# Optimization experiments

Hardware: AMD Instinct MI355X
Metric: run time of the kernel (lower is better)

Reference implementation:

```python
import jax, jax.numpy as jnp
import numpy as np

B, T, N, C_IN, C_OUT, D_E, GH, H = 16, 12, 2048, 64, 64, 16, 32, 4


def setup_inputs() -> dict:
    key = jax.random.key(0)
    ks = jax.random.split(key, 12)
    f = jax.random.normal
    return {
        "x": f(ks[0], (B, T, N, C_IN), jnp.float32),
        "init_state": jnp.zeros((B, N, C_OUT), jnp.float32),
        "node_embeddings": f(ks[1], (N, D_E), jnp.float32),
        "gat_W": f(ks[2], (H, D_E, GH), jnp.float32) * 0.3,
        "gat_a_src": f(ks[3], (H, GH), jnp.float32) * 0.3,
        "gat_a_dst": f(ks[4], (H, GH), jnp.float32) * 0.3,
        "wp_gates": f(ks[5], (D_E, 2, C_IN + C_OUT, 2 * C_OUT), jnp.float32) * 0.05,
        "bp_gates": f(ks[6], (D_E, 2 * C_OUT), jnp.float32) * 0.05,
        "wp_cand": f(ks[7], (D_E, 2, C_IN + C_OUT, C_OUT), jnp.float32) * 0.05,
        "bp_cand": f(ks[8], (D_E, C_OUT), jnp.float32) * 0.05,
        "tc_w": f(ks[9], (C_OUT, C_OUT, 1, 3), jnp.float32) * 0.05,
        "tc_b": jnp.zeros((C_OUT,), jnp.float32),
        "rc_w": f(ks[10], (C_OUT, C_IN, 1, 1), jnp.float32) * 0.05,
        "rc_b": jnp.zeros((C_OUT,), jnp.float32),
        "ln_g": jnp.ones((C_OUT,), jnp.float32),
        "ln_b": jnp.zeros((C_OUT,), jnp.float32),
    }


def _forward(x, init_state, node_embeddings, gat_W, gat_a_src, gat_a_dst,
             wp_gates, bp_gates, wp_cand, bp_cand, tc_w, tc_b, rc_w, rc_b, ln_g, ln_b):
    E = node_embeddings
    # GAT-style adaptive support over node embeddings: [N, N]
    h = jnp.einsum('nd,hdf->hnf', E, gat_W)                       # [H,N,GH]
    s = jnp.einsum('hnf,hf->hn', h, gat_a_src)
    d = jnp.einsum('hnf,hf->hn', h, gat_a_dst)
    e = jax.nn.leaky_relu(s[:, :, None] + d[:, None, :], 0.2)     # [H,N,N]
    A = jax.nn.softmax(e, axis=-1).mean(0)                        # [N,N]
    # node-adaptive weights (NAL): per-node weights from embedding pools
    W_g = jnp.einsum('nd,dkio->nkio', E, wp_gates)                # [N,2,Cin+Cout,2Cout]
    b_g = E @ bp_gates                                            # [N,2Cout]
    W_c = jnp.einsum('nd,dkio->nkio', E, wp_cand)
    b_c = E @ bp_cand

    def gconv(inp, W, b):
        # cheb order-2 supports [I, A] over inp: [B,N,C] -> [B,N,out]
        xg = jnp.stack([inp, jnp.einsum('mn,bnc->bmc', A, inp)], 2)
        return jnp.einsum('bnki,nkio->bno', xg, W) + b

    def step(state, xt):
        zr = jax.nn.sigmoid(gconv(jnp.concatenate([xt, state], -1), W_g, b_g))
        z, r = jnp.split(zr, 2, axis=-1)
        hc = jnp.tanh(gconv(jnp.concatenate([xt, r * state], -1), W_c, b_c))
        new = z * state + (1.0 - z) * hc
        return new, new

    last, inner = jax.lax.scan(step, init_state, jnp.swapaxes(x, 0, 1))
    inner = jnp.swapaxes(inner, 0, 1)                             # [B,T,N,C]

    cur = jnp.transpose(inner, (0, 3, 2, 1))                      # [B,C,N,T]
    tco = jax.lax.conv_general_dilated(
        cur, tc_w, (1, 1), [(0, 0), (1, 1)],
        dimension_numbers=('NCHW', 'OIHW', 'NCHW')) + tc_b[None, :, None, None]
    xp = jnp.transpose(x, (0, 3, 2, 1))                           # [B,Cin,N,T]
    res = jnp.einsum('oc,bcnt->bont', rc_w[:, :, 0, 0], xp) + rc_b[None, :, None, None]
    y = jnp.transpose(jax.nn.relu(res + tco), (0, 3, 2, 1))       # [B,T,N,C]
    mu = y.mean(-1, keepdims=True)
    var = y.var(-1, keepdims=True)
    y = (y - mu) / jnp.sqrt(var + 1e-5) * ln_g + ln_b
    return y, last


def reference(x, init_state, node_embeddings, gat_W, gat_a_src, gat_a_dst,
              wp_gates, bp_gates, wp_cand, bp_cand, tc_w, tc_b, rc_w, rc_b, ln_g, ln_b):
    y, last = _forward(x, init_state, node_embeddings, gat_W, gat_a_src, gat_a_dst,
                       wp_gates, bp_gates, wp_cand, bp_cand, tc_w, tc_b, rc_w, rc_b, ln_g, ln_b)
    return (y, last)
```

## Files before the change

### kernel.cpp

```cpp
#include <hip/hip_runtime.h>
#include <stdint.h>

#define B_  16
#define T_  12
#define N_  2048
#define DE_ 16
#define GH_ 32
#define NH_ 4

typedef __attribute__((ext_vector_type(8)))  short short8;
typedef __attribute__((ext_vector_type(4)))  float f32x4;
typedef __attribute__((ext_vector_type(16))) float f32x16;

__device__ __forceinline__ unsigned short f2b(float f){
  unsigned u = __float_as_uint(f);
  return (unsigned short)((u + 0x7fffu + ((u>>16)&1u)) >> 16);
}
__device__ __forceinline__ float b2f(unsigned short h){
  return __uint_as_float(((unsigned)h)<<16);
}
__device__ __forceinline__ unsigned pk2(float a, float b){
  return (unsigned)f2b(a) | ((unsigned)f2b(b)<<16);
}
__device__ __forceinline__ float lrelu(float v){ return v>=0.f ? v : 0.2f*v; }

__device__ __forceinline__ void gl16(const void* g, void* l){
  __builtin_amdgcn_global_load_lds((const __attribute__((address_space(1))) void*)g,
                                   (__attribute__((address_space(3))) void*)l, 16, 0, 0);
}

__global__ __launch_bounds__(256) void k_gat_sd(const float* __restrict__ E, const float* __restrict__ gW,
    const float* __restrict__ asrc, const float* __restrict__ adst,
    float* __restrict__ sArr, float* __restrict__ dArr)
{
  int id = blockIdx.x*256 + threadIdx.x;
  int h = id >> 11, n = id & 2047;
  float hv[GH_];
#pragma unroll
  for (int f=0; f<GH_; ++f) hv[f]=0.f;
  for (int d=0; d<DE_; ++d){
    float e = E[n*DE_+d];
    const float* wr = gW + (h*DE_+d)*GH_;
#pragma unroll
    for (int f=0; f<GH_; ++f) hv[f] += e*wr[f];
  }
  float s=0.f, dd=0.f;
#pragma unroll
  for (int f=0; f<GH_; ++f){ s += hv[f]*asrc[h*GH_+f]; dd += hv[f]*adst[h*GH_+f]; }
  sArr[h*N_+n]=s; dArr[h*N_+n]=dd;
}

__global__ __launch_bounds__(256) void k_dmax(const float* __restrict__ dArr, float* __restrict__ dmax){
  __shared__ float red[256];
  int h = blockIdx.x, t = threadIdx.x;
  float m = -1e30f;
  for (int i=t;i<N_;i+=256) m = fmaxf(m, dArr[h*N_+i]);
  red[t]=m; __syncthreads();
  for (int s=128;s>0;s>>=1){ if (t<s) red[t]=fmaxf(red[t],red[t+s]); __syncthreads(); }
  if (t==0) dmax[h]=red[0];
}

__global__ __launch_bounds__(256) void k_denom(const float* __restrict__ sArr, const float* __restrict__ dArr,
                                               const float* __restrict__ dmax, float* __restrict__ denom){
  __shared__ float red[256];
  int m = blockIdx.x, h = blockIdx.y, t = threadIdx.x;
  float sm = sArr[h*N_+m];
  float shift = lrelu(sm + dmax[h]);
  float acc=0.f;
  for (int i=t;i<N_;i+=256) acc += __expf(lrelu(sm + dArr[h*N_+i]) - shift);
  red[t]=acc; __syncthreads();
  for (int s=128;s>0;s>>=1){ if (t<s) red[t]+=red[t+s]; __syncthreads(); }
  if (t==0) denom[h*N_+m]=red[0];
}

__global__ __launch_bounds__(256) void k_adj(const float* __restrict__ sArr, const float* __restrict__ dArr,
                                             const float* __restrict__ dmax, const float* __restrict__ denom,
                                             unsigned short* __restrict__ Abf){
  int m = blockIdx.x, t = threadIdx.x;
  float sm[NH_], sh[NH_], inv[NH_];
#pragma unroll
  for (int h=0;h<NH_;++h){ sm[h]=sArr[h*N_+m]; sh[h]=lrelu(sm[h]+dmax[h]); inv[h]=1.f/denom[h*N_+m]; }
  for (int n=t;n<N_;n+=256){
    float acc=0.f;
#pragma unroll
    for (int h=0;h<NH_;++h) acc += __expf(lrelu(sm[h]+dArr[h*N_+n]) - sh[h]) * inv[h];
    Abf[(long)m*N_+n] = f2b(acc*0.25f);
  }
}

__global__ __launch_bounds__(256) void k_nalw(const float* __restrict__ E, const float* __restrict__ wp,
                                              unsigned short* __restrict__ Wout, int Osz){
  __shared__ float sS[256][17];
  __shared__ float sE[512*16];
  int o = blockIdx.x, q = blockIdx.y, t = threadIdx.x;
  int slot = t>>3, j = t&7;
  int kio = (((slot ^ (o&7))&31)<<3) | j;
  long dstride = 256L*Osz;
  for (int d=0; d<DE_; ++d) sS[t][d] = wp[d*dstride + (long)kio*Osz + o];
  for (int i=t; i<512*16; i+=256) sE[i] = E[q*512*16 + i];
  __syncthreads();
  unsigned short* out = Wout + (long)(q*512)*dstride + o*256 + t;
  for (int nn=0; nn<512; ++nn){
    float acc=0.f;
    const float* e = &sE[nn*16];
#pragma unroll
    for (int d=0; d<DE_; ++d) acc += e[d]*sS[t][d];
    out[(long)nn*dstride] = f2b(acc);
  }
}

__global__ __launch_bounds__(256) void k_nalb(const float* __restrict__ E, const float* __restrict__ bpg,
                                              const float* __restrict__ bpc,
                                              unsigned short* __restrict__ bg, unsigned short* __restrict__ bc){
  int id = blockIdx.x*256+threadIdx.x;
  int n = id/192, oo = id%192;
  float acc=0.f;
  if (oo<128){
    for (int d=0;d<DE_;++d) acc += E[n*DE_+d]*bpg[d*128+oo];
    bg[n*128+oo]=f2b(acc);
  } else {
    int c=oo-128;
    for (int d=0;d<DE_;++d) acc += E[n*DE_+d]*bpc[d*64+c];
    bc[n*64+c]=f2b(acc);
  }
}

__global__ __launch_bounds__(256) void k_wcat(const float* __restrict__ tcw, const float* __restrict__ rcw,
                                              unsigned short* __restrict__ Wcat){
  int id = blockIdx.x*256+threadIdx.x;
  int o = id>>8, k = id&255;
  float v;
  if (k<192){ int dt=k>>6, c=k&63; v = tcw[(o*64+c)*3+dt]; }
  else v = rcw[o*64 + (k&63)];
  int pos = o*256 + ((((k>>3)&31) ^ (o&7))<<3) + (k&7);
  Wcat[pos] = f2b(v);
}

__global__ __launch_bounds__(256) void k_init(const float* __restrict__ init, float* __restrict__ st,
                                              unsigned short* __restrict__ stb){
  int i = blockIdx.x*256+threadIdx.x;
  float v = init[i]; st[i]=v; stb[i]=f2b(v);
}

template<int BM, int BN, bool F32SRC>
__global__ __launch_bounds__(256) void k_gemm(
    const unsigned short* __restrict__ Abf,
    const char* __restrict__ S0, long ss0,
    const char* __restrict__ S1, long ss1,
    unsigned short* __restrict__ D0, long ds0,
    unsigned short* __restrict__ D1, long ds1)
{
  constexpr int BK=64;
  constexpr int IA = BM/32;
  constexpr int WTM = BM/2, WTN = BN/2;
  constexpr int MTC = WTM/32, NTC = WTN/32;
  __shared__ __align__(16) unsigned short sA[BM*BK];
  __shared__ __align__(16) unsigned short sB[BN*BK];
  int tid = threadIdx.x, w = tid>>6, l = tid&63;
  int mB = blockIdx.x, z = blockIdx.y;
  const char* s0 = S0 + (long)z*ss0;
  const char* s1 = (BN==128) ? (S1 + (long)z*ss1) : (const char*)0;
  int wm = w&1, wn = w>>1;
  f32x16 acc[MTC][NTC];
#pragma unroll
  for (int a=0;a<MTC;++a)
#pragma unroll
    for (int b=0;b<NTC;++b)
#pragma unroll
      for (int i=0;i<16;++i) acc[a][b][i]=0.f;

  constexpr int JG = BN/4;
  int jg = tid & (JG-1), kg = tid / JG;
  bool bact = (kg < 8);
  int j0 = jg*4, k0 = kg*8;

  for (int kb=0; kb<2048/BK; ++kb){
    __syncthreads();
#pragma unroll
    for (int i=0;i<IA;++i){
      int c = (w*IA+i)*64 + l;
      int row = c>>3, slot = c&7;
      int g = slot ^ (row&7);
      gl16((const char*)Abf + (((long)(mB*BM+row))*2048 + kb*BK + g*8)*2,
           (char*)sA + (w*IA+i)*1024);
    }
    if (bact){
      unsigned short vv[8][4];
#pragma unroll
      for (int ii=0; ii<8; ++ii){
        int k = kb*BK + k0 + ii;
        const char* sp; int jj0;
        if (BN==128 && j0>=64){ sp = s1; jj0 = j0-64; } else { sp = s0; jj0 = j0; }
        if (F32SRC){
          const float4 v = *(const float4*)(sp + ((long)k*64 + jj0)*4);
          vv[ii][0]=f2b(v.x); vv[ii][1]=f2b(v.y); vv[ii][2]=f2b(v.z); vv[ii][3]=f2b(v.w);
        } else {
          const ushort4 v = *(const ushort4*)(sp + ((long)k*64 + jj0)*2);
          vv[ii][0]=v.x; vv[ii][1]=v.y; vv[ii][2]=v.z; vv[ii][3]=v.w;
        }
      }
#pragma unroll
      for (int r=0;r<4;++r){
        int jj = j0 + r;
        uint4 pkv;
        pkv.x = (unsigned)vv[0][r] | ((unsigned)vv[1][r]<<16);
        pkv.y = (unsigned)vv[2][r] | ((unsigned)vv[3][r]<<16);
        pkv.z = (unsigned)vv[4][r] | ((unsigned)vv[5][r]<<16);
        pkv.w = (unsigned)vv[6][r] | ((unsigned)vv[7][r]<<16);
        *(uint4*)((char*)sB + jj*128 + ((kg ^ (jj&7))<<4)) = pkv;
      }
    }
    __syncthreads();
#pragma unroll
    for (int ks=0; ks<BK/16; ++ks){
      short8 af[MTC];
#pragma unroll
      for (int mt=0; mt<MTC; ++mt){
        int row = wm*WTM + mt*32 + (l&31);
        int g = ks*2 + (l>>5);
        af[mt] = *(const short8*)((const char*)sA + row*128 + ((g ^ (row&7))<<4));
      }
#pragma unroll
      for (int nt=0; nt<NTC; ++nt){
        int jj = wn*WTN + nt*32 + (l&31);
        int g = ks*2 + (l>>5);
        short8 bfv = *(const short8*)((const char*)sB + jj*128 + ((g ^ (jj&7))<<4));
#pragma unroll
        for (int mt=0; mt<MTC; ++mt)
          acc[mt][nt] = __builtin_amdgcn_mfma_f32_32x32x16_bf16(af[mt], bfv, acc[mt][nt], 0,0,0);
      }
    }
  }
  unsigned short* d0 = D0 + (long)z*ds0;
  unsigned short* d1 = (BN==128) ? (D1 + (long)z*ds1) : (unsigned short*)0;
#pragma unroll
  for (int mt=0; mt<MTC; ++mt)
#pragma unroll
    for (int nt=0; nt<NTC; ++nt)
#pragma unroll
      for (int rg=0; rg<16; ++rg){
        int rl = wm*WTM + mt*32 + (rg&3) + 8*(rg>>2) + 4*(l>>5);
        int col = wn*WTN + nt*32 + (l&31);
        long m = (long)mB*BM + rl;
        unsigned short v = f2b(acc[mt][nt][rg]);
        if (BN==128 && col>=64) d1[m*64 + (col-64)] = v;
        else d0[m*64 + col] = v;
      }
}

__global__ __launch_bounds__(256) void k_gates(
    const float* __restrict__ x, const float* __restrict__ st,
    const unsigned short* __restrict__ AX, const unsigned short* __restrict__ AS,
    const unsigned short* __restrict__ Wg, const unsigned short* __restrict__ bg,
    float* __restrict__ zbuf, unsigned short* __restrict__ rs, int t)
{
  __shared__ __align__(16) unsigned short sW[64*256];
  __shared__ __align__(16) unsigned short sX[16*256];
  int n = blockIdx.x, half = blockIdx.y;
  int tid = threadIdx.x, w = tid>>6, l = tid&63;
  const unsigned short* Wsrc = Wg + (long)n*32768 + half*16384;
#pragma unroll
  for (int i=0;i<8;++i){
    int c = (w*8+i)*64 + l;
    gl16((const char*)Wsrc + c*16, (char*)sW + (w*8+i)*1024);
  }
  int b = tid>>4, c16 = tid&15;
  uint4 g0, g1;
  if (c16 < 8){
    const float* p = (c16<4) ? (x  + (((long)(b*T_+t)*N_ + n)*64 + c16*16))
                             : (st + (((long)b*N_ + n)*64 + (c16-4)*16));
    float4 f0 = *(const float4*)(p+0), f1 = *(const float4*)(p+4);
    float4 f2v = *(const float4*)(p+8), f3 = *(const float4*)(p+12);
    g0.x = pk2(f0.x,f0.y); g0.y = pk2(f0.z,f0.w); g0.z = pk2(f1.x,f1.y); g0.w = pk2(f1.z,f1.w);
    g1.x = pk2(f2v.x,f2v.y); g1.y = pk2(f2v.z,f2v.w); g1.z = pk2(f3.x,f3.y); g1.w = pk2(f3.z,f3.w);
  } else {
    const unsigned short* p = (c16<12) ? (AX + (((long)(b*T_+t)*N_ + n)*64 + (c16-8)*16))
                                       : (AS + (((long)b*N_ + n)*64 + (c16-12)*16));
    g0 = *(const uint4*)(p); g1 = *(const uint4*)(p+8);
  }
  {
    int gg = c16*2;
    *(uint4*)((char*)sX + b*512 + (((gg  ) ^ (b&7))<<4)) = g0;
    *(uint4*)((char*)sX + b*512 + (((gg+1) ^ (b&7))<<4)) = g1;
  }
  __syncthreads();
  f32x4 acc; 
#pragma unroll
  for (int i=0;i<4;++i) acc[i]=0.f;
  int orow = w*16 + (l&15);
  int arow = l&15;
#pragma unroll
  for (int ks=0; ks<8; ++ks){
    int g = ks*4 + (l>>4);
    short8 a = *(const short8*)((const char*)sX + arow*512 + ((g ^ (arow&7))<<4));
    short8 bb = *(const short8*)((const char*)sW + orow*512 + ((g ^ (orow&7))<<4));
    acc = __builtin_amdgcn_mfma_f32_16x16x32_bf16(a, bb, acc, 0,0,0);
  }
  int o = half*64 + orow;
  float bia = b2f(bg[n*128 + o]);
#pragma unroll
  for (int i=0;i<4;++i){
    int bb2 = (l>>4)*4 + i;
    float v = acc[i] + bia;
    float sg = 1.f/(1.f+__expf(-v));
    long idx = ((long)bb2*N_ + n)*64;
    if (half==0) zbuf[idx + o] = sg;
    else {
      float s0v = st[idx + (o-64)];
      rs[idx + (o-64)] = f2b(sg*s0v);
    }
  }
}

__global__ __launch_bounds__(256) void k_cand(
    const float* __restrict__ x, const float* __restrict__ zbuf,
    const unsigned short* __restrict__ AX, const unsigned short* __restrict__ ARS,
    const unsigned short* __restrict__ rs,
    const unsigned short* __restrict__ Wc, const unsigned short* __restrict__ bc,
    float* __restrict__ st, unsigned short* __restrict__ stb,
    unsigned short* __restrict__ inner, int t)
{
  __shared__ __align__(16) unsigned short sW[64*256];
  __shared__ __align__(16) unsigned short sX[16*256];
  int n = blockIdx.x;
  int tid = threadIdx.x, w = tid>>6, l = tid&63;
  const unsigned short* Wsrc = Wc + (long)n*16384;
#pragma unroll
  for (int i=0;i<8;++i){
    int c = (w*8+i)*64 + l;
    gl16((const char*)Wsrc + c*16, (char*)sW + (w*8+i)*1024);
  }
  int b = tid>>4, c16 = tid&15;
  uint4 g0, g1;
  if (c16 < 4){
    const float* p = x + (((long)(b*T_+t)*N_ + n)*64 + c16*16);
    float4 f0 = *(const float4*)(p+0), f1 = *(const float4*)(p+4);
    float4 f2v = *(const float4*)(p+8), f3 = *(const float4*)(p+12);
    g0.x = pk2(f0.x,f0.y); g0.y = pk2(f0.z,f0.w); g0.z = pk2(f1.x,f1.y); g0.w = pk2(f1.z,f1.w);
    g1.x = pk2(f2v.x,f2v.y); g1.y = pk2(f2v.z,f2v.w); g1.z = pk2(f3.x,f3.y); g1.w = pk2(f3.z,f3.w);
  } else {
    const unsigned short* p;
    if (c16<8)       p = rs  + (((long)b*N_ + n)*64 + (c16-4)*16);
    else if (c16<12) p = AX  + (((long)(b*T_+t)*N_ + n)*64 + (c16-8)*16);
    else             p = ARS + (((long)b*N_ + n)*64 + (c16-12)*16);
    g0 = *(const uint4*)(p); g1 = *(const uint4*)(p+8);
  }
  {
    int gg = c16*2;
    *(uint4*)((char*)sX + b*512 + (((gg  ) ^ (b&7))<<4)) = g0;
    *(uint4*)((char*)sX + b*512 + (((gg+1) ^ (b&7))<<4)) = g1;
  }
  __syncthreads();
  f32x4 acc;
#pragma unroll
  for (int i=0;i<4;++i) acc[i]=0.f;
  int orow = w*16 + (l&15);
  int arow = l&15;
#pragma unroll
  for (int ks=0; ks<8; ++ks){
    int g = ks*4 + (l>>4);
    short8 a = *(const short8*)((const char*)sX + arow*512 + ((g ^ (arow&7))<<4));
    short8 bb = *(const short8*)((const char*)sW + orow*512 + ((g ^ (orow&7))<<4));
    acc = __builtin_amdgcn_mfma_f32_16x16x32_bf16(a, bb, acc, 0,0,0);
  }
  float bia = b2f(bc[n*64 + orow]);
#pragma unroll
  for (int i=0;i<4;++i){
    int bb2 = (l>>4)*4 + i;
    float hc = tanhf(acc[i] + bia);
    long idx = ((long)bb2*N_ + n)*64 + orow;
    float zv = zbuf[idx];
    float olds = st[idx];
    float nv = zv*olds + (1.f-zv)*hc;
    st[idx]=nv; stb[idx]=f2b(nv);
    inner[((long)(bb2*T_+t)*N_ + n)*64 + orow] = f2b(nv);
  }
}

__global__ __launch_bounds__(256) void k_post(
    const unsigned short* __restrict__ inner, const float* __restrict__ x,
    const unsigned short* __restrict__ Wcat,
    const float* __restrict__ tcb, const float* __restrict__ rcb,
    const float* __restrict__ lng, const float* __restrict__ lnb,
    float* __restrict__ out)
{
  __shared__ __align__(16) unsigned short sF[64*256];
  __shared__ __align__(16) unsigned short sW[64*256];
  int id = blockIdx.x;
  int bt = id>>5, nb = id&31;
  int b = bt/T_, t = bt%T_;
  int n0 = nb*64;
  int tid = threadIdx.x, w = tid>>6, l = tid&63;
#pragma unroll
  for (int i=0;i<8;++i){
    int c = (w*8+i)*64 + l;
    gl16((const char*)Wcat + c*16, (char*)sW + (w*8+i)*1024);
  }
  int row = tid&63, q = tid>>6;
  uint4 ch[8];
  if (q<3){
    int ts = t + q - 1;
    if (ts>=0 && ts<T_){
      const uint4* p = (const uint4*)(inner + (((long)(b*T_+ts)*N_) + n0+row)*64);
#pragma unroll
      for (int hh=0;hh<8;++hh) ch[hh]=p[hh];
    } else {
      uint4 zz; zz.x=0u; zz.y=0u; zz.z=0u; zz.w=0u;
#pragma unroll
      for (int hh=0;hh<8;++hh) ch[hh]=zz;
    }
  } else {
    const float4* p = (const float4*)(x + (((long)bt*N_) + n0+row)*64);
#pragma unroll
    for (int hh=0;hh<8;++hh){
      float4 u0=p[2*hh], u1=p[2*hh+1];
      ch[hh].x=pk2(u0.x,u0.y); ch[hh].y=pk2(u0.z,u0.w);
      ch[hh].z=pk2(u1.x,u1.y); ch[hh].w=pk2(u1.z,u1.w);
    }
  }
#pragma unroll
  for (int hh=0;hh<8;++hh){
    int g = q*8+hh;
    *(uint4*)((char*)sF + row*512 + ((g ^ (row&7))<<4)) = ch[hh];
  }
  __syncthreads();
  f32x4 acc[4];
#pragma unroll
  for (int ot=0; ot<4; ++ot)
#pragma unroll
    for (int i=0;i<4;++i) acc[ot][i]=0.f;
  int arow = w*16 + (l&15);
#pragma unroll
  for (int ks=0; ks<8; ++ks){
    int g = ks*4 + (l>>4);
    short8 a = *(const short8*)((const char*)sF + arow*512 + ((g ^ (arow&7))<<4));
#pragma unroll
    for (int ot=0; ot<4; ++ot){
      int o = ot*16 + (l&15);
      short8 bb = *(const short8*)((const char*)sW + o*512 + ((g ^ (o&7))<<4));
      acc[ot] = __builtin_amdgcn_mfma_f32_16x16x32_bf16(a, bb, acc[ot], 0,0,0);
    }
  }
  float s1[4]={0.f,0.f,0.f,0.f}, s2[4]={0.f,0.f,0.f,0.f};
#pragma unroll
  for (int ot=0; ot<4; ++ot){
    int o = ot*16 + (l&15);
    float bia = tcb[o] + rcb[o];
#pragma unroll
    for (int i=0;i<4;++i){
      float v = fmaxf(acc[ot][i] + bia, 0.f);
      acc[ot][i] = v;
      s1[i]+=v; s2[i]+=v*v;
    }
  }
#pragma unroll
  for (int msk=1; msk<16; msk<<=1){
#pragma unroll
    for (int i=0;i<4;++i){
      s1[i] += __shfl_xor(s1[i], msk, 64);
      s2[i] += __shfl_xor(s2[i], msk, 64);
    }
  }
#pragma unroll
  for (int i=0;i<4;++i){
    float mu = s1[i]*(1.f/64.f);
    float var = s2[i]*(1.f/64.f) - mu*mu;
    float rstd = rsqrtf(fmaxf(var,0.f)+1e-5f);
    int rr = n0 + w*16 + (l>>4)*4 + i;
#pragma unroll
    for (int ot=0; ot<4; ++ot){
      int o = ot*16 + (l&15);
      out[(((long)bt*N_) + rr)*64 + o] = (acc[ot][i]-mu)*rstd*lng[o] + lnb[o];
    }
  }
}

extern "C" void kernel_launch(void* const* d_in, const int* in_sizes, int n_in,
                              void* d_out, int out_size, void* d_ws, size_t ws_size,
                              hipStream_t stream)
{
  const float* x    = (const float*)d_in[0];
  const float* init = (const float*)d_in[1];
  const float* E    = (const float*)d_in[2];
  const float* gW   = (const float*)d_in[3];
  const float* asrc = (const float*)d_in[4];
  const float* adst = (const float*)d_in[5];
  const float* wpg  = (const float*)d_in[6];
  const float* bpg  = (const float*)d_in[7];
  const float* wpc  = (const float*)d_in[8];
  const float* bpc  = (const float*)d_in[9];
  const float* tcw  = (const float*)d_in[10];
  const float* tcb  = (const float*)d_in[11];
  const float* rcw  = (const float*)d_in[12];
  const float* rcb  = (const float*)d_in[13];
  const float* lng  = (const float*)d_in[14];
  const float* lnb  = (const float*)d_in[15];
  float* out = (float*)d_out;

  char* p = (char*)d_ws;
  auto alloc = [&](size_t bytes)->char*{ char* r = p; p += (bytes + 255) & ~(size_t)255; return r; };
  unsigned short* Abf  = (unsigned short*)alloc((size_t)N_*N_*2);
  unsigned short* Wg   = (unsigned short*)alloc((size_t)N_*32768*2);
  unsigned short* Wc   = (unsigned short*)alloc((size_t)N_*16384*2);
  unsigned short* bg   = (unsigned short*)alloc((size_t)N_*128*2);
  unsigned short* bc   = (unsigned short*)alloc((size_t)N_*64*2);
  unsigned short* AX   = (unsigned short*)alloc((size_t)B_*T_*N_*64*2);
  unsigned short* AS   = (unsigned short*)alloc((size_t)B_*N_*64*2);
  unsigned short* ARS  = (unsigned short*)alloc((size_t)B_*N_*64*2);
  unsigned short* rsb  = (unsigned short*)alloc((size_t)B_*N_*64*2);
  unsigned short* stb  = (unsigned short*)alloc((size_t)B_*N_*64*2);
  unsigned short* inner= (unsigned short*)alloc((size_t)B_*T_*N_*64*2);
  unsigned short* Wcat = (unsigned short*)alloc((size_t)64*256*2);
  float* sArr = (float*)alloc((size_t)NH_*N_*4);
  float* dArr = (float*)alloc((size_t)NH_*N_*4);
  float* dmax = (float*)alloc((size_t)NH_*4);
  float* denom= (float*)alloc((size_t)NH_*N_*4);
  float* stf  = (float*)alloc((size_t)B_*N_*64*4);
  float* zbuf = (float*)alloc((size_t)B_*N_*64*4);

  k_gat_sd<<<32,256,0,stream>>>(E,gW,asrc,adst,sArr,dArr);
  k_dmax<<<4,256,0,stream>>>(dArr,dmax);
  k_denom<<<dim3(N_,NH_),256,0,stream>>>(sArr,dArr,dmax,denom);
  k_adj<<<N_,256,0,stream>>>(sArr,dArr,dmax,denom,Abf);
  k_nalw<<<dim3(128,4),256,0,stream>>>(E,wpg,Wg,128);
  k_nalw<<<dim3(64,4),256,0,stream>>>(E,wpc,Wc,64);
  k_nalb<<<1536,256,0,stream>>>(E,bpg,bpc,bg,bc);
  k_wcat<<<64,256,0,stream>>>(tcw,rcw,Wcat);
  k_init<<<(B_*N_*64)/256,256,0,stream>>>(init,stf,stb);

  k_gemm<128,128,true><<<dim3(16,96),256,0,stream>>>(Abf,
      (const char*)x,          2L*N_*64*4,
      (const char*)(x + N_*64),2L*N_*64*4,
      AX,          2L*N_*64,
      AX + N_*64,  2L*N_*64);

  for (int t=0; t<T_; ++t){
    k_gemm<64,64,false><<<dim3(32,16),256,0,stream>>>(Abf,
        (const char*)stb, (long)N_*64*2, (const char*)0, 0,
        AS, (long)N_*64, (unsigned short*)0, 0);
    k_gates<<<dim3(N_,2),256,0,stream>>>(x,stf,AX,AS,Wg,bg,zbuf,rsb,t);
    k_gemm<64,64,false><<<dim3(32,16),256,0,stream>>>(Abf,
        (const char*)rsb, (long)N_*64*2, (const char*)0, 0,
        ARS, (long)N_*64, (unsigned short*)0, 0);
    k_cand<<<N_,256,0,stream>>>(x,zbuf,AX,ARS,rsb,Wc,bc,stf,stb,inner,t);
  }

  k_post<<<B_*T_*32,256,0,stream>>>(inner,x,Wcat,tcb,rcb,lng,lnb,out);
  hipMemcpyAsync(out + (size_t)B_*T_*N_*64, stf, (size_t)B_*N_*64*4,
                 hipMemcpyDeviceToDevice, stream);
}
```

Measured before the change: 2.073 ms.

## Pre-swizzle GEMM B operands so A·X GEMMs load B tiles directly

Adds a pre-pass that converts x to bf16 in a k-blocked, XOR-swizzled layout. The state and reset-state producers now also write that layout, so the adjacency GEMMs can fetch B tiles with direct 16-byte global-to-LDS loads instead of doing per-thread transposes and conversions. The GEMM outputs switch to a node-major layout with all batches side by side, so one wide GEMM covers all B*T or B columns. Blocks are also remapped so that neighbouring M tiles land on the same XCD. In exchange there are extra buffers, an extra swizzled write of rs, and scattered stores in the gate and candidate epilogues.

```diff
diff --git a/kernel.cpp b/kernel.cpp
--- a/kernel.cpp
+++ b/kernel.cpp
@@ -86,6 +86,37 @@
     for (int h=0;h<NH_;++h) acc += __expf(lrelu(sm[h]+dArr[h*N_+n]) - sh[h]) * inv[h];
     Abf[(long)m*N_+n] = f2b(acc*0.25f);
   }
+}
+
+__global__ __launch_bounds__(256) void k_xsw(const float* __restrict__ x,
+                                             unsigned short* __restrict__ xsw)
+{
+  __shared__ unsigned short sT[256*64];
+  int kb = blockIdx.x;
+  int btB = blockIdx.y;
+  int tid = threadIdx.x;
+  int btl = tid>>6, kin = tid&63;
+  int n  = kb*64 + kin;
+  int bt = btB*4 + btl;
+  const float* src = x + ((long)bt*N_ + n)*64;
+  unsigned short row[64];
+#pragma unroll
+  for (int c4=0; c4<16; ++c4){
+    float4 v = *(const float4*)(src + c4*4);
+    row[c4*4+0]=f2b(v.x); row[c4*4+1]=f2b(v.y); row[c4*4+2]=f2b(v.z); row[c4*4+3]=f2b(v.w);
+  }
+  int g0 = kin>>3, e = kin&7;
+#pragma unroll
+  for (int c=0; c<64; ++c){
+    int jl = btl*64 + c;
+    int s = g0 ^ (c&7);
+    sT[jl*64 + s*8 + e] = row[c];
+  }
+  __syncthreads();
+  unsigned short* dst = xsw + ((long)kb*12288 + btB*256)*64;
+  const uint4* sp = (const uint4*)sT;
+  uint4* dp = (uint4*)dst;
+  for (int i=tid; i<2048; i+=256) dp[i] = sp[i];
 }
 
 __global__ __launch_bounds__(256) void k_nalw(const float* __restrict__ E, const float* __restrict__ wp,
@@ -136,30 +167,35 @@
   Wcat[pos] = f2b(v);
 }
 
-__global__ __launch_bounds__(256) void k_init(const float* __restrict__ init, float* __restrict__ st,
-                                              unsigned short* __restrict__ stb){
+__global__ __launch_bounds__(256) void k_init2(const float* __restrict__ init, float* __restrict__ st,
+                                               unsigned short* __restrict__ stb){
   int i = blockIdx.x*256+threadIdx.x;
-  float v = init[i]; st[i]=v; stb[i]=f2b(v);
-}
-
-template<int BM, int BN, bool F32SRC>
-__global__ __launch_bounds__(256) void k_gemm(
-    const unsigned short* __restrict__ Abf,
-    const char* __restrict__ S0, long ss0,
-    const char* __restrict__ S1, long ss1,
-    unsigned short* __restrict__ D0, long ds0,
-    unsigned short* __restrict__ D1, long ds1)
-{
-  constexpr int BK=64;
-  constexpr int IA = BM/32;
+  float v = init[i]; st[i]=v;
+  int c = i&63, n = (i>>6)&2047, b = i>>17;
+  int kb = n>>6, kin = n&63;
+  int j = b*64 + c;
+  int s = (kin>>3) ^ (c&7);
+  stb[((long)kb*1024 + j)*64 + s*8 + (kin&7)] = f2b(v);
+}
+
+template<int BM, int BN, int JTOT>
+__global__ __launch_bounds__(256) void k_gemm2(
+    const unsigned short* __restrict__ A,
+    const unsigned short* __restrict__ Bs,
+    unsigned short* __restrict__ D)
+{
+  constexpr int MBLK = 2048/BM, MPX = MBLK/8;
+  constexpr int NIA = BM*64*2/(256*16);
+  constexpr int NIB = BN*64*2/(256*16);
   constexpr int WTM = BM/2, WTN = BN/2;
   constexpr int MTC = WTM/32, NTC = WTN/32;
-  __shared__ __align__(16) unsigned short sA[BM*BK];
-  __shared__ __align__(16) unsigned short sB[BN*BK];
+  __shared__ __align__(16) unsigned short sA[BM*64];
+  __shared__ __align__(16) unsigned short sB[BN*64];
+  int bid = blockIdx.x;
+  int xcd = bid & 7, idx = bid >> 3;
+  int mB = xcd*MPX + (idx % MPX);
+  int jB = idx / MPX;
   int tid = threadIdx.x, w = tid>>6, l = tid&63;
-  int mB = blockIdx.x, z = blockIdx.y;
-  const char* s0 = S0 + (long)z*ss0;
-  const char* s1 = (BN==128) ? (S1 + (long)z*ss1) : (const char*)0;
   int wm = w&1, wn = w>>1;
   f32x16 acc[MTC][NTC];
 #pragma unroll
@@ -169,70 +205,39 @@
 #pragma unroll
       for (int i=0;i<16;++i) acc[a][b][i]=0.f;
 
-  constexpr int JG = BN/4;
-  int jg = tid & (JG-1), kg = tid / JG;
-  bool bact = (kg < 8);
-  int j0 = jg*4, k0 = kg*8;
-
-  for (int kb=0; kb<2048/BK; ++kb){
+  for (int kb=0; kb<32; ++kb){
     __syncthreads();
 #pragma unroll
-    for (int i=0;i<IA;++i){
-      int c = (w*IA+i)*64 + l;
-      int row = c>>3, slot = c&7;
-      int g = slot ^ (row&7);
-      gl16((const char*)Abf + (((long)(mB*BM+row))*2048 + kb*BK + g*8)*2,
-           (char*)sA + (w*IA+i)*1024);
-    }
-    if (bact){
-      unsigned short vv[8][4];
-#pragma unroll
-      for (int ii=0; ii<8; ++ii){
-        int k = kb*BK + k0 + ii;
-        const char* sp; int jj0;
-        if (BN==128 && j0>=64){ sp = s1; jj0 = j0-64; } else { sp = s0; jj0 = j0; }
-        if (F32SRC){
-          const float4 v = *(const float4*)(sp + ((long)k*64 + jj0)*4);
-          vv[ii][0]=f2b(v.x); vv[ii][1]=f2b(v.y); vv[ii][2]=f2b(v.z); vv[ii][3]=f2b(v.w);
-        } else {
-          const ushort4 v = *(const ushort4*)(sp + ((long)k*64 + jj0)*2);
-          vv[ii][0]=v.x; vv[ii][1]=v.y; vv[ii][2]=v.z; vv[ii][3]=v.w;
-        }
-      }
-#pragma unroll
-      for (int r=0;r<4;++r){
-        int jj = j0 + r;
-        uint4 pkv;
-        pkv.x = (unsigned)vv[0][r] | ((unsigned)vv[1][r]<<16);
-        pkv.y = (unsigned)vv[2][r] | ((unsigned)vv[3][r]<<16);
-        pkv.z = (unsigned)vv[4][r] | ((unsigned)vv[5][r]<<16);
-        pkv.w = (unsigned)vv[6][r] | ((unsigned)vv[7][r]<<16);
-        *(uint4*)((char*)sB + jj*128 + ((kg ^ (jj&7))<<4)) = pkv;
-      }
-    }
+    for (int i=0;i<NIA;++i){
+      int c = (w*NIA+i)*64 + l;
+      int row = c>>3, slot = c&7, g = slot ^ (row&7);
+      gl16((const char*)A + (((long)(mB*BM+row))*2048 + kb*64 + g*8)*2,
+           (char*)sA + (w*NIA+i)*1024);
+    }
+    const char* bt = (const char*)(Bs + ((long)kb*JTOT + jB*BN)*64);
+#pragma unroll
+    for (int i=0;i<NIB;++i)
+      gl16(bt + ((w*NIB+i)*64 + l)*16, (char*)sB + (w*NIB+i)*1024);
     __syncthreads();
 #pragma unroll
-    for (int ks=0; ks<BK/16; ++ks){
+    for (int ks=0; ks<4; ++ks){
+      int gk = ks*2 + (l>>5);
       short8 af[MTC];
 #pragma unroll
       for (int mt=0; mt<MTC; ++mt){
         int row = wm*WTM + mt*32 + (l&31);
-        int g = ks*2 + (l>>5);
-        af[mt] = *(const short8*)((const char*)sA + row*128 + ((g ^ (row&7))<<4));
+        af[mt] = *(const short8*)((const char*)sA + row*128 + ((gk ^ (row&7))<<4));
       }
 #pragma unroll
       for (int nt=0; nt<NTC; ++nt){
         int jj = wn*WTN + nt*32 + (l&31);
-        int g = ks*2 + (l>>5);
-        short8 bfv = *(const short8*)((const char*)sB + jj*128 + ((g ^ (jj&7))<<4));
+        short8 bfv = *(const short8*)((const char*)sB + jj*128 + ((gk ^ (jj&7))<<4));
 #pragma unroll
         for (int mt=0; mt<MTC; ++mt)
           acc[mt][nt] = __builtin_amdgcn_mfma_f32_32x32x16_bf16(af[mt], bfv, acc[mt][nt], 0,0,0);
       }
     }
   }
-  unsigned short* d0 = D0 + (long)z*ds0;
-  unsigned short* d1 = (BN==128) ? (D1 + (long)z*ds1) : (unsigned short*)0;
 #pragma unroll
   for (int mt=0; mt<MTC; ++mt)
 #pragma unroll
@@ -240,19 +245,18 @@
 #pragma unroll
       for (int rg=0; rg<16; ++rg){
         int rl = wm*WTM + mt*32 + (rg&3) + 8*(rg>>2) + 4*(l>>5);
-        int col = wn*WTN + nt*32 + (l&31);
+        int col = jB*BN + wn*WTN + nt*32 + (l&31);
         long m = (long)mB*BM + rl;
-        unsigned short v = f2b(acc[mt][nt][rg]);
-        if (BN==128 && col>=64) d1[m*64 + (col-64)] = v;
-        else d0[m*64 + col] = v;
+        D[m*JTOT + col] = f2b(acc[mt][nt][rg]);
       }
 }
 
 __global__ __launch_bounds__(256) void k_gates(
     const float* __restrict__ x, const float* __restrict__ st,
-    const unsigned short* __restrict__ AX, const unsigned short* __restrict__ AS,
+    const unsigned short* __restrict__ AXn, const unsigned short* __restrict__ AS,
     const unsigned short* __restrict__ Wg, const unsigned short* __restrict__ bg,
-    float* __restrict__ zbuf, unsigned short* __restrict__ rs, int t)
+    float* __restrict__ zbuf, unsigned short* __restrict__ rsp,
+    unsigned short* __restrict__ rsb, int t)
 {
   __shared__ __align__(16) unsigned short sW[64*256];
   __shared__ __align__(16) unsigned short sX[16*256];
@@ -274,8 +278,9 @@
     g0.x = pk2(f0.x,f0.y); g0.y = pk2(f0.z,f0.w); g0.z = pk2(f1.x,f1.y); g0.w = pk2(f1.z,f1.w);
     g1.x = pk2(f2v.x,f2v.y); g1.y = pk2(f2v.z,f2v.w); g1.z = pk2(f3.x,f3.y); g1.w = pk2(f3.z,f3.w);
   } else {
-    const unsigned short* p = (c16<12) ? (AX + (((long)(b*T_+t)*N_ + n)*64 + (c16-8)*16))
-                                       : (AS + (((long)b*N_ + n)*64 + (c16-12)*16));
+    const unsigned short* p = (c16<12)
+      ? (AXn + ((long)n*12288 + (b*T_+t)*64 + (c16-8)*16))
+      : (AS  + ((long)n*1024  + b*64       + (c16-12)*16));
     g0 = *(const uint4*)(p); g1 = *(const uint4*)(p+8);
   }
   {
@@ -284,7 +289,7 @@
     *(uint4*)((char*)sX + b*512 + (((gg+1) ^ (b&7))<<4)) = g1;
   }
   __syncthreads();
-  f32x4 acc; 
+  f32x4 acc;
 #pragma unroll
   for (int i=0;i<4;++i) acc[i]=0.f;
   int orow = w*16 + (l&15);
@@ -298,24 +303,28 @@
   }
   int o = half*64 + orow;
   float bia = b2f(bg[n*128 + o]);
+  int kb = n>>6, kin = n&63;
+  int sw = (kin>>3) ^ (orow&7);
 #pragma unroll
   for (int i=0;i<4;++i){
-    int bb2 = (l>>4)*4 + i;
+    int b2 = (l>>4)*4 + i;
     float v = acc[i] + bia;
     float sg = 1.f/(1.f+__expf(-v));
-    long idx = ((long)bb2*N_ + n)*64;
+    long idx = ((long)b2*N_ + n)*64;
     if (half==0) zbuf[idx + o] = sg;
     else {
-      float s0v = st[idx + (o-64)];
-      rs[idx + (o-64)] = f2b(sg*s0v);
+      float s0v = st[idx + orow];
+      unsigned short rv = f2b(sg*s0v);
+      rsp[idx + orow] = rv;
+      rsb[((long)kb*1024 + b2*64 + orow)*64 + sw*8 + (kin&7)] = rv;
     }
   }
 }
 
 __global__ __launch_bounds__(256) void k_cand(
     const float* __restrict__ x, const float* __restrict__ zbuf,
-    const unsigned short* __restrict__ AX, const unsigned short* __restrict__ ARS,
-    const unsigned short* __restrict__ rs,
+    const unsigned short* __restrict__ AXn, const unsigned short* __restrict__ ARS,
+    const unsigned short* __restrict__ rsp,
     const unsigned short* __restrict__ Wc, const unsigned short* __restrict__ bc,
     float* __restrict__ st, unsigned short* __restrict__ stb,
     unsigned short* __restrict__ inner, int t)
@@ -340,9 +349,9 @@
     g1.x = pk2(f2v.x,f2v.y); g1.y = pk2(f2v.z,f2v.w); g1.z = pk2(f3.x,f3.y); g1.w = pk2(f3.z,f3.w);
   } else {
     const unsigned short* p;
-    if (c16<8)       p = rs  + (((long)b*N_ + n)*64 + (c16-4)*16);
-    else if (c16<12) p = AX  + (((long)(b*T_+t)*N_ + n)*64 + (c16-8)*16);
-    else             p = ARS + (((long)b*N_ + n)*64 + (c16-12)*16);
+    if (c16<8)       p = rsp + (((long)b*N_ + n)*64 + (c16-4)*16);
+    else if (c16<12) p = AXn + ((long)n*12288 + (b*T_+t)*64 + (c16-8)*16);
+    else             p = ARS + ((long)n*1024  + b*64       + (c16-12)*16);
     g0 = *(const uint4*)(p); g1 = *(const uint4*)(p+8);
   }
   {
@@ -364,16 +373,20 @@
     acc = __builtin_amdgcn_mfma_f32_16x16x32_bf16(a, bb, acc, 0,0,0);
   }
   float bia = b2f(bc[n*64 + orow]);
+  int kb = n>>6, kin = n&63;
+  int sw = (kin>>3) ^ (orow&7);
 #pragma unroll
   for (int i=0;i<4;++i){
-    int bb2 = (l>>4)*4 + i;
+    int b2 = (l>>4)*4 + i;
     float hc = tanhf(acc[i] + bia);
-    long idx = ((long)bb2*N_ + n)*64 + orow;
+    long idx = ((long)b2*N_ + n)*64 + orow;
     float zv = zbuf[idx];
     float olds = st[idx];
     float nv = zv*olds + (1.f-zv)*hc;
-    st[idx]=nv; stb[idx]=f2b(nv);
-    inner[((long)(bb2*T_+t)*N_ + n)*64 + orow] = f2b(nv);
+    st[idx]=nv;
+    unsigned short nb = f2b(nv);
+    stb[((long)kb*1024 + b2*64 + orow)*64 + sw*8 + (kin&7)] = nb;
+    inner[((long)(b2*T_+t)*N_ + n)*64 + orow] = nb;
   }
 }
 
@@ -504,11 +517,13 @@
   unsigned short* Wc   = (unsigned short*)alloc((size_t)N_*16384*2);
   unsigned short* bg   = (unsigned short*)alloc((size_t)N_*128*2);
   unsigned short* bc   = (unsigned short*)alloc((size_t)N_*64*2);
-  unsigned short* AX   = (unsigned short*)alloc((size_t)B_*T_*N_*64*2);
-  unsigned short* AS   = (unsigned short*)alloc((size_t)B_*N_*64*2);
-  unsigned short* ARS  = (unsigned short*)alloc((size_t)B_*N_*64*2);
-  unsigned short* rsb  = (unsigned short*)alloc((size_t)B_*N_*64*2);
-  unsigned short* stb  = (unsigned short*)alloc((size_t)B_*N_*64*2);
+  unsigned short* xsw  = (unsigned short*)alloc((size_t)N_*12288*2);
+  unsigned short* AXn  = (unsigned short*)alloc((size_t)N_*12288*2);
+  unsigned short* AS   = (unsigned short*)alloc((size_t)N_*1024*2);
+  unsigned short* ARS  = (unsigned short*)alloc((size_t)N_*1024*2);
+  unsigned short* rsb  = (unsigned short*)alloc((size_t)N_*1024*2);
+  unsigned short* rsp  = (unsigned short*)alloc((size_t)N_*1024*2);
+  unsigned short* stb  = (unsigned short*)alloc((size_t)N_*1024*2);
   unsigned short* inner= (unsigned short*)alloc((size_t)B_*T_*N_*64*2);
   unsigned short* Wcat = (unsigned short*)alloc((size_t)64*256*2);
   float* sArr = (float*)alloc((size_t)NH_*N_*4);
@@ -522,27 +537,20 @@
   k_dmax<<<4,256,0,stream>>>(dArr,dmax);
   k_denom<<<dim3(N_,NH_),256,0,stream>>>(sArr,dArr,dmax,denom);
   k_adj<<<N_,256,0,stream>>>(sArr,dArr,dmax,denom,Abf);
+  k_xsw<<<dim3(32,48),256,0,stream>>>(x,xsw);
   k_nalw<<<dim3(128,4),256,0,stream>>>(E,wpg,Wg,128);
   k_nalw<<<dim3(64,4),256,0,stream>>>(E,wpc,Wc,64);
   k_nalb<<<1536,256,0,stream>>>(E,bpg,bpc,bg,bc);
   k_wcat<<<64,256,0,stream>>>(tcw,rcw,Wcat);
-  k_init<<<(B_*N_*64)/256,256,0,stream>>>(init,stf,stb);
-
-  k_gemm<128,128,true><<<dim3(16,96),256,0,stream>>>(Abf,
-      (const char*)x,          2L*N_*64*4,
-      (const char*)(x + N_*64),2L*N_*64*4,
-      AX,          2L*N_*64,
-      AX + N_*64,  2L*N_*64);
+  k_init2<<<(B_*N_*64)/256,256,0,stream>>>(init,stf,stb);
+
+  k_gemm2<128,128,12288><<<1536,256,0,stream>>>(Abf, xsw, AXn);
 
   for (int t=0; t<T_; ++t){
-    k_gemm<64,64,false><<<dim3(32,16),256,0,stream>>>(Abf,
-        (const char*)stb, (long)N_*64*2, (const char*)0, 0,
-        AS, (long)N_*64, (unsigned short*)0, 0);
-    k_gates<<<dim3(N_,2),256,0,stream>>>(x,stf,AX,AS,Wg,bg,zbuf,rsb,t);
-    k_gemm<64,64,false><<<dim3(32,16),256,0,stream>>>(Abf,
-        (const char*)rsb, (long)N_*64*2, (const char*)0, 0,
-        ARS, (long)N_*64, (unsigned short*)0, 0);
-    k_cand<<<N_,256,0,stream>>>(x,zbuf,AX,ARS,rsb,Wc,bc,stf,stb,inner,t);
+    k_gemm2<64,64,1024><<<512,256,0,stream>>>(Abf, stb, AS);
+    k_gates<<<dim3(N_,2),256,0,stream>>>(x,stf,AXn,AS,Wg,bg,zbuf,rsp,rsb,t);
+    k_gemm2<64,64,1024><<<512,256,0,stream>>>(Abf, rsb, ARS);
+    k_cand<<<N_,256,0,stream>>>(x,zbuf,AXn,ARS,rsp,Wc,bc,stf,stb,inner,t);
   }
 
   k_post<<<B_*T_*32,256,0,stream>>>(inner,x,Wcat,tcb,rcb,lng,lnb,out);
```

Measured after the change: 2.102 ms. About the same (+1.4%).
